# Kernel tuning notes

Hardware: AMD Instinct MI355X
Metric: run time of the kernel (lower is better)

Reference implementation:

```python
import jax, jax.numpy as jnp
import numpy as np

EPS_BN = 1e-3  # nn.BatchNorm1d(num_channels, eps=0.001)
B, C, N = 16, 256, 2048
NUM_SA = 4


def _bn(x, g, b, m, v):
    # eval-mode BatchNorm1d over channel dim of [B, C, N]
    return g[:, None] * (x - m[:, None]) * jax.lax.rsqrt(v[:, None] + EPS_BN) + b[:, None]


def _sa_layer(x, qk_w, v_w, v_b, t_w, t_b, g, b, m, var):
    # q_conv and k_conv share weights -> energy = (Wx)^T (Wx)
    q = jnp.einsum('oc,bcn->bon', qk_w, x)              # [B, C//4, N]
    energy = jnp.einsum('bcm,bcn->bmn', q, q)           # [B, N, N]
    attn = jax.nn.softmax(energy, axis=-1)
    # offset-attention: extra column-sum normalization (dim=1)
    attn = attn / (1e-9 + attn.sum(axis=1, keepdims=True))
    xv = jnp.einsum('oc,bcn->bon', v_w, x) + v_b[:, None]   # [B, C, N]
    x_r = jnp.einsum('bcn,bnm->bcm', xv, attn)              # bmm(x_v, attention)
    t = jnp.einsum('oc,bcn->bon', t_w, x - x_r) + t_b[:, None]
    return x + jax.nn.relu(_bn(t, g, b, m, var))


def setup_inputs() -> dict:
    key = jax.random.key(0)
    ks = jax.random.split(key, 24)
    f32 = jnp.float32
    d = {}
    d['x'] = jax.random.normal(ks[0], (B, C, N), dtype=f32)
    d['conv1_w'] = jax.random.normal(ks[1], (C, C), dtype=f32) * 0.05
    d['conv2_w'] = jax.random.normal(ks[2], (C, C), dtype=f32) * 0.05
    for i, nm in enumerate(['bn1', 'bn2']):
        kk = jax.random.split(ks[3 + i], 4)
        d[nm + '_g'] = 1.0 + 0.05 * jax.random.normal(kk[0], (C,), dtype=f32)
        d[nm + '_b'] = 0.05 * jax.random.normal(kk[1], (C,), dtype=f32)
        d[nm + '_m'] = 0.05 * jax.random.normal(kk[2], (C,), dtype=f32)
        d[nm + '_v'] = jax.random.uniform(kk[3], (C,), dtype=f32, minval=0.5, maxval=1.5)
    d['sa_qk_w'] = jax.random.normal(ks[5], (NUM_SA, C // 4, C), dtype=f32) * 0.05
    d['sa_v_w'] = jax.random.normal(ks[6], (NUM_SA, C, C), dtype=f32) * 0.05
    d['sa_v_b'] = jax.random.normal(ks[7], (NUM_SA, C), dtype=f32) * 0.05
    d['sa_t_w'] = jax.random.normal(ks[8], (NUM_SA, C, C), dtype=f32) * 0.05
    d['sa_t_b'] = jax.random.normal(ks[9], (NUM_SA, C), dtype=f32) * 0.05
    d['sa_g'] = 1.0 + 0.05 * jax.random.normal(ks[10], (NUM_SA, C), dtype=f32)
    d['sa_b'] = 0.05 * jax.random.normal(ks[11], (NUM_SA, C), dtype=f32)
    d['sa_m'] = 0.05 * jax.random.normal(ks[12], (NUM_SA, C), dtype=f32)
    d['sa_var'] = jax.random.uniform(ks[13], (NUM_SA, C), dtype=f32, minval=0.5, maxval=1.5)
    d['flag'] = 0  # False -> primary bn branch
    return d


def reference(x, conv1_w, conv2_w, bn1_g, bn1_b, bn1_m, bn1_v,
              bn2_g, bn2_b, bn2_m, bn2_v,
              sa_qk_w, sa_v_w, sa_v_b, sa_t_w, sa_t_b,
              sa_g, sa_b, sa_m, sa_var, flag):
    h = jax.nn.relu(_bn(jnp.einsum('oc,bcn->bon', conv1_w, x), bn1_g, bn1_b, bn1_m, bn1_v))
    h = jax.nn.relu(_bn(jnp.einsum('oc,bcn->bon', conv2_w, h), bn2_g, bn2_b, bn2_m, bn2_v))
    outs = []
    for i in range(NUM_SA):
        h = _sa_layer(h, sa_qk_w[i], sa_v_w[i], sa_v_b[i], sa_t_w[i], sa_t_b[i],
                      sa_g[i], sa_b[i], sa_m[i], sa_var[i])
        outs.append(h)
    return jnp.concatenate(outs, axis=1)  # [B, 4*C, N]
```

## Files before the change

### kernel.cpp

```cpp
#include <hip/hip_runtime.h>
#include <hip/hip_bf16.h>
#include <hip/hip_fp16.h>

static constexpr int Bn = 16;
static constexpr int Cc = 256;
static constexpr int Nn = 2048;
static constexpr int C4 = 64;
static constexpr float LOG2E = 1.4426950408889634f;

typedef _Float16 half_t;
typedef __attribute__((ext_vector_type(8))) _Float16 half8;
typedef __attribute__((ext_vector_type(4))) _Float16 half4;
typedef __attribute__((ext_vector_type(8))) short short8;
typedef __attribute__((ext_vector_type(4))) float float4v;

static constexpr long sNC = (long)Nn * Cc;
static constexpr long sNQ = (long)Nn * C4;

#define DEVI __device__ __forceinline__

DEVI float bf2f(unsigned short u) { return __uint_as_float(((unsigned)u) << 16); }
DEVI unsigned short f2bf(float f) {
    unsigned x = __float_as_uint(f);
    x += 0x7fffu + ((x >> 16) & 1u);
    return (unsigned short)(x >> 16);
}

DEVI void gload16(const void* g, void* l) {
    __builtin_amdgcn_global_load_lds(
        (const __attribute__((address_space(1))) unsigned int*)g,
        (__attribute__((address_space(3))) unsigned int*)l, 16, 0, 0);
}

enum { EPI_RAW = 0, EPI_H = 1, EPI_XV = 2 };

template<int MODE, int BM, int BN, int WI, int WJ, bool BF16OUT>
__global__ __launch_bounds__(WI * WJ * 64)
void mgemm(const half_t* __restrict__ A, long aB,
           const half_t* __restrict__ Bm, long bB,
           void* __restrict__ Yv, long yB, int ldy,
           const float* __restrict__ bias,
           const float* __restrict__ bng, const float* __restrict__ bnb,
           const float* __restrict__ bnm, const float* __restrict__ bnv,
           int K,
           const float* __restrict__ Pbuf, float* __restrict__ offp)
{
    constexpr int NW = WI * WJ;
    __shared__ __align__(16) half_t Als[2][BM][32];
    __shared__ __align__(16) half_t Bls[2][BN][32];

    const int tid  = threadIdx.x;
    const int w    = tid >> 6;
    const int lane = tid & 63;
    const int wi   = w % WI;
    const int wj   = w / WI;
    const int quad = lane >> 4, m16 = lane & 15;
    const int lr   = lane >> 2, lc = lane & 3;
    const int b    = blockIdx.z;
    const int j0   = blockIdx.x * BN;
    const int i0   = blockIdx.y * BM;

    const half_t* Ab = A + (size_t)b * aB;
    const half_t* Bb = Bm + (size_t)b * bB;

    float4v acc[4][4];
    #pragma unroll
    for (int i = 0; i < 4; ++i)
        #pragma unroll
        for (int j = 0; j < 4; ++j) acc[i][j] = (float4v)0.f;

    bool first = true;
    for (int k0 = 0; k0 < K; k0 += 64) {
        #pragma unroll
        for (int s = 0; s < 2; ++s) {
            const int kk = k0 + s * 32 + lc * 8;
            #pragma unroll
            for (int t = 0; t < BM / (16 * NW); ++t) {
                const int row = (t * NW + w) * 16;
                gload16(Ab + (size_t)(i0 + row + lr) * K + kk, &Als[s][row][0]);
            }
            #pragma unroll
            for (int t = 0; t < BN / (16 * NW); ++t) {
                const int row = (t * NW + w) * 16;
                gload16(Bb + (size_t)(j0 + row + lr) * K + kk, &Bls[s][row][0]);
            }
        }
        if (MODE == EPI_XV && first && Pbuf && tid < 128) {
            const int m = blockIdx.y * 128 + tid;
            const float2* p = (const float2*)(Pbuf + ((size_t)b * Nn + m) * 32);
            float M = -1e30f;
            #pragma unroll
            for (int i = 0; i < 16; ++i) M = fmaxf(M, p[i].x);
            float S = 0.f;
            #pragma unroll
            for (int i = 0; i < 16; ++i) S += p[i].y * __expf(p[i].x - M);
            offp[(size_t)b * Nn + m] = fmaf(M, LOG2E, __log2f(S));
        }
        first = false;
        __syncthreads();
        #pragma unroll
        for (int s = 0; s < 2; ++s) {
            half8 af[4], bf[4];
            #pragma unroll
            for (int t = 0; t < 4; ++t)
                af[t] = *(const half8*)&Als[s][wi * 64 + t * 16 + m16][quad * 8];
            #pragma unroll
            for (int t = 0; t < 4; ++t)
                bf[t] = *(const half8*)&Bls[s][wj * 64 + t * 16 + m16][quad * 8];
            #pragma unroll
            for (int ti = 0; ti < 4; ++ti)
                #pragma unroll
                for (int tj = 0; tj < 4; ++tj)
                    acc[ti][tj] = __builtin_amdgcn_mfma_f32_16x16x32_f16(
                        af[ti], bf[tj], acc[ti][tj], 0, 0, 0);
        }
        __syncthreads();
    }

    #pragma unroll
    for (int ti = 0; ti < 4; ++ti) {
        const int il = i0 + wi * 64 + ti * 16 + quad * 4;
        #pragma unroll
        for (int tj = 0; tj < 4; ++tj) {
            const int jl = j0 + wj * 64 + tj * 16 + m16;
            float4v v = acc[ti][tj];
            if (MODE == EPI_RAW) {
                half4 o;
                #pragma unroll
                for (int r = 0; r < 4; ++r) o[r] = (half_t)v[r];
                *(half4*)((half_t*)Yv + (size_t)b * yB + (size_t)jl * ldy + il) = o;
            } else if (MODE == EPI_H) {
                half4 o;
                #pragma unroll
                for (int r = 0; r < 4; ++r) {
                    const float sc = bng[il + r] * rsqrtf(bnv[il + r] + 1e-3f);
                    const float sh = bnb[il + r] - bnm[il + r] * sc;
                    o[r] = (half_t)fmaxf(fmaf(v[r], sc, sh), 0.f);
                }
                *(half4*)((half_t*)Yv + (size_t)b * yB + (size_t)jl * ldy + il) = o;
            } else {
                const float bj = bias[jl];
                if (BF16OUT) {
                    ushort4 o;
                    o.x = f2bf(v[0] + bj); o.y = f2bf(v[1] + bj);
                    o.z = f2bf(v[2] + bj); o.w = f2bf(v[3] + bj);
                    *(ushort4*)((unsigned short*)Yv + (size_t)b * yB + (size_t)jl * ldy + il) = o;
                } else {
                    half4 o;
                    #pragma unroll
                    for (int r = 0; r < 4; ++r) o[r] = (half_t)(v[r] + bj);
                    *(half4*)((half_t*)Yv + (size_t)b * yB + (size_t)jl * ldy + il) = o;
                }
            }
        }
    }
}

__global__ __launch_bounds__(256)
void estats(const half_t* __restrict__ q, float* __restrict__ Pbuf)
{
    __shared__ __align__(16) half_t sA[128 * 64];
    __shared__ __align__(16) half_t sB[128 * 64];
    __shared__ float red[2][2][4][16][2];
    const int tid = threadIdx.x, w = tid >> 6, lane = tid & 63;
    const int wi = w & 1, wj = w >> 1, quad = lane >> 4, m16 = lane & 15;
    const int f = blockIdx.x;
    const int W = (f & 7) * 512 + (f >> 3);
    const int b = W >> 8;
    const int rem = W & 255;
    const int j0 = (rem & 15) * 128;
    const int ib = rem >> 4;
    const int i0 = ib * 128;
    const half_t* qb = q + (size_t)b * sNQ;

    #pragma unroll
    for (int t = 0; t < 4; ++t) {
        const int g = w * 256 + t * 64 + lane;
        const int r = g >> 3, c = g & 7;
        const int cs = c ^ (r & 7);
        gload16(qb + (size_t)(i0 + r) * 64 + cs * 8, sA + (w * 256 + t * 64) * 8);
        gload16(qb + (size_t)(j0 + r) * 64 + cs * 8, sB + (w * 256 + t * 64) * 8);
    }
    __syncthreads();

    half8 an[4][2], bm[4][2];
    #pragma unroll
    for (int t = 0; t < 4; ++t)
        #pragma unroll
        for (int ks = 0; ks < 2; ++ks) {
            const int pc = ((ks * 4 + quad) ^ (m16 & 7)) * 8;
            an[t][ks] = *(const half8*)&sA[(wi * 64 + t * 16 + m16) * 64 + pc];
            bm[t][ks] = *(const half8*)&sB[(wj * 64 + t * 16 + m16) * 64 + pc];
        }

    #pragma unroll
    for (int tj = 0; tj < 4; ++tj) {
        float4v e[4];
        #pragma unroll
        for (int ti = 0; ti < 4; ++ti) {
            e[ti] = (float4v)0.f;
            e[ti] = __builtin_amdgcn_mfma_f32_16x16x32_f16(an[ti][0], bm[tj][0], e[ti], 0, 0, 0);
            e[ti] = __builtin_amdgcn_mfma_f32_16x16x32_f16(an[ti][1], bm[tj][1], e[ti], 0, 0, 0);
        }
        float lmax = -1e30f;
        #pragma unroll
        for (int ti = 0; ti < 4; ++ti)
            #pragma unroll
            for (int r = 0; r < 4; ++r) lmax = fmaxf(lmax, e[ti][r]);
        lmax = fmaxf(lmax, __shfl_xor(lmax, 16));
        lmax = fmaxf(lmax, __shfl_xor(lmax, 32));
        float ls = 0.f;
        #pragma unroll
        for (int ti = 0; ti < 4; ++ti)
            #pragma unroll
            for (int r = 0; r < 4; ++r) ls += __expf(e[ti][r] - lmax);
        ls += __shfl_xor(ls, 16);
        ls += __shfl_xor(ls, 32);
        if (quad == 0) { red[wi][wj][tj][m16][0] = lmax; red[wi][wj][tj][m16][1] = ls; }
    }
    __syncthreads();
    if (tid < 128) {
        const int wj2 = tid >> 6, tj2 = (tid >> 4) & 3, mm = tid & 15;
        const float m0 = red[0][wj2][tj2][mm][0], s0 = red[0][wj2][tj2][mm][1];
        const float m1 = red[1][wj2][tj2][mm][0], s1 = red[1][wj2][tj2][mm][1];
        const float M = fmaxf(m0, m1);
        const float S = s0 * __expf(m0 - M) + s1 * __expf(m1 - M);
        const int m = j0 + wj2 * 64 + tj2 * 16 + mm;
        *(float2*)(Pbuf + (((size_t)b * Nn + m) * 16 + ib) * 2) = make_float2(M, S);
    }
}

__global__ __launch_bounds__(512)
void flashxr(const half_t* __restrict__ q, const half_t* __restrict__ xv,
             const half_t* __restrict__ h, const float* __restrict__ offp,
             const half_t* __restrict__ tw, const float* __restrict__ tb,
             const float* __restrict__ bng, const float* __restrict__ bnb,
             const float* __restrict__ bnm, const float* __restrict__ bnv,
             float* __restrict__ outL, half_t* __restrict__ hNext,
             const half_t* __restrict__ qkn, half_t* __restrict__ qn)
{
    __shared__ __align__(16) half_t sXV[256 * 64];
    __shared__ __align__(16) half_t sQA[2][64 * 64];
    __shared__ __align__(16) half_t sP[64 * 64];
    __shared__ float sOff[Nn];

    const int tid = threadIdx.x, w = tid >> 6, lane = tid & 63;
    const int quad = lane >> 4, m16 = lane & 15;
    const int wiE = w & 1, wjE = w >> 1;
    const int wi = w & 3, wj = w >> 2;
    const int wjT = w;
    const int f = blockIdx.x;
    const int W = (f & 7) * 64 + (f >> 3);
    const int b = W >> 5, j0 = (W & 31) * 64;
    const half_t* qb  = q + (size_t)b * sNQ;
    const half_t* xvb = xv + (size_t)b * sNC;

    const int sr = tid >> 3, sc = tid & 7;
    const int qsw = (sc ^ (sr & 7)) * 8;

    gload16(qb + (size_t)sr * 64 + qsw, &sQA[0][(size_t)tid * 8]);
    gload16(offp + (size_t)b * Nn + (size_t)tid * 4, sOff + (size_t)tid * 4);

    half8 bq[2];
    #pragma unroll
    for (int s = 0; s < 2; ++s)
        bq[s] = *(const half8*)(qb + (size_t)(j0 + wjE * 16 + m16) * 64 + (s * 4 + quad) * 8);

    __syncthreads();

    float4v acc[4][2];
    #pragma unroll
    for (int i = 0; i < 4; ++i)
        #pragma unroll
        for (int j = 0; j < 2; ++j) acc[i][j] = (float4v)0.f;
    float csa = 0.f;
    const int mrow = wjE * 16 + m16;

    for (int nc = 0; nc < 32; ++nc) {
        #pragma unroll
        for (int t = 0; t < 4; ++t) {
            const int g = t * 512 + tid;
            const int r = g >> 3, c = g & 7;
            gload16(xvb + (size_t)r * Nn + nc * 64 + ((c ^ (r & 7)) * 8),
                    sXV + (size_t)g * 8);
        }
        if (nc < 31)
            gload16(qb + (size_t)((nc + 1) * 64 + sr) * 64 + qsw,
                    &sQA[(nc + 1) & 1][(size_t)tid * 8]);
        __syncthreads();

        const half_t* qA = &sQA[nc & 1][0];
        const int nbase = nc * 64 + wiE * 32 + quad * 4;
        #pragma unroll
        for (int ti = 0; ti < 2; ++ti) {
            const int nl = wiE * 32 + ti * 16 + m16;
            const half8 an0 = *(const half8*)&qA[(size_t)nl * 64 + ((quad ^ (m16 & 7)) * 8)];
            const half8 an1 = *(const half8*)&qA[(size_t)nl * 64 + (((4 + quad) ^ (m16 & 7)) * 8)];
            float4v e = (float4v)0.f;
            e = __builtin_amdgcn_mfma_f32_16x16x32_f16(an0, bq[0], e, 0, 0, 0);
            e = __builtin_amdgcn_mfma_f32_16x16x32_f16(an1, bq[1], e, 0, 0, 0);
            const float4v o4 = *(const float4v*)&sOff[nbase + ti * 16];
            float c0 = 0.f; ushort4 pk;
            #pragma unroll
            for (int r = 0; r < 4; ++r) {
                const float p = __builtin_amdgcn_exp2f(fmaf(e[r], LOG2E, -o4[r]));
                c0 += p; (&pk.x)[r] = f2bf(p);
            }
            csa += c0;
            const int pc = (wiE * 4 + ti * 2 + (quad >> 1)) ^ (m16 & 7);
            *(ushort4*)&((unsigned short*)sP)[(size_t)mrow * 64 + pc * 8 + (quad & 1) * 4] = pk;
        }
        __syncthreads();

        #pragma unroll
        for (int ks = 0; ks < 2; ++ks) {
            short8 xa[4], pb[2];
            #pragma unroll
            for (int ti = 0; ti < 4; ++ti)
                xa[ti] = *(const short8*)&sXV[(size_t)(wi * 64 + ti * 16 + m16) * 64
                                              + (((ks * 4 + quad) ^ (m16 & 7)) * 8)];
            #pragma unroll
            for (int tj = 0; tj < 2; ++tj)
                pb[tj] = *(const short8*)&sP[(size_t)(wj * 32 + tj * 16 + m16) * 64
                                             + (((ks * 4 + quad) ^ (m16 & 7)) * 8)];
            __builtin_amdgcn_s_setprio(1);
            #pragma unroll
            for (int ti = 0; ti < 4; ++ti)
                #pragma unroll
                for (int tj = 0; tj < 2; ++tj)
                    acc[ti][tj] = __builtin_amdgcn_mfma_f32_16x16x32_bf16(
                        xa[ti], pb[tj], acc[ti][tj], 0, 0, 0);
            __builtin_amdgcn_s_setprio(0);
        }
        __syncthreads();
    }

    csa += __shfl_xor(csa, 16);
    csa += __shfl_xor(csa, 32);
    float* fb = (float*)sP;
    if (lane < 16) fb[wiE * 64 + wjE * 16 + lane] = csa;
    __syncthreads();
    float csr[2];
    #pragma unroll
    for (int tj = 0; tj < 2; ++tj) {
        const int m = wj * 32 + tj * 16 + m16;
        csr[tj] = 1.0f / (1e-9f + fb[m] + fb[64 + m]);
    }

    const half_t* hb = h + (size_t)b * sNC;
    half_t* sD = sXV;
    #pragma unroll
    for (int ti = 0; ti < 4; ++ti) {
        const int cg = wi * 64 + ti * 16 + quad * 4;
        const int cc = (cg >> 3) ^ (m16 & 7);
        const int sub = (quad & 1) * 4;
        #pragma unroll
        for (int tj = 0; tj < 2; ++tj) {
            const int mr = wj * 32 + tj * 16 + m16;
            const int mg = j0 + mr;
            const half4 hv = *(const half4*)&hb[(size_t)mg * Cc + cg];
            half4 o;
            #pragma unroll
            for (int r = 0; r < 4; ++r)
                o[r] = (half_t)((float)hv[r] - acc[ti][tj][r] * csr[tj]);
            *(half4*)&sD[(size_t)mr * 256 + cc * 8 + sub] = o;
        }
    }
    __syncthreads();

    float4v acc2[4][2];
    #pragma unroll
    for (int i = 0; i < 4; ++i)
        #pragma unroll
        for (int j = 0; j < 2; ++j) acc2[i][j] = (float4v)0.f;
    #pragma unroll
    for (int ks = 0; ks < 8; ++ks) {
        half8 af[4], bf[2];
        #pragma unroll
        for (int tm = 0; tm < 4; ++tm)
            af[tm] = *(const half8*)&sD[(size_t)(tm * 16 + m16) * 256
                                        + (((ks * 4 + quad) ^ (m16 & 7)) * 8)];
        #pragma unroll
        for (int tc = 0; tc < 2; ++tc)
            bf[tc] = *(const half8*)&tw[(size_t)(wjT * 32 + tc * 16 + m16) * 256
                                        + ks * 32 + quad * 8];
        #pragma unroll
        for (int tm = 0; tm < 4; ++tm)
            #pragma unroll
            for (int tc = 0; tc < 2; ++tc)
                acc2[tm][tc] = __builtin_amdgcn_mfma_f32_16x16x32_f16(
                    af[tm], bf[tc], acc2[tm][tc], 0, 0, 0);
    }

    if (qn) __syncthreads();

    half_t* sH = sXV;
    const long yB = (long)4 * Cc * Nn;
    float* yb = outL + (size_t)b * yB;
    half_t* hn = hNext ? hNext + (size_t)b * sNC : nullptr;
    #pragma unroll
    for (int tc = 0; tc < 2; ++tc) {
        const int co = wjT * 32 + tc * 16 + m16;
        const float tb2 = tb[co];
        const float sc2 = bng[co] * rsqrtf(bnv[co] + 1e-3f);
        const float sh2 = bnb[co] - bnm[co] * sc2;
        #pragma unroll
        for (int tm = 0; tm < 4; ++tm) {
            const int mg = j0 + tm * 16 + quad * 4;
            float4v o;
            #pragma unroll
            for (int r = 0; r < 4; ++r) {
                const float t2  = acc2[tm][tc][r] + tb2;
                const float rel = fmaxf(fmaf(t2, sc2, sh2), 0.f);
                const float hv  = (float)hb[(size_t)(mg + r) * Cc + co];
                const float ov  = hv + rel;
                o[r] = ov;
                if (hn) hn[(size_t)(mg + r) * Cc + co] = (half_t)ov;
                if (qn) {
                    const int row = tm * 16 + quad * 4 + r;
                    const int chk = ((co >> 3) ^ (row & 7));
                    sH[(size_t)row * 256 + chk * 8 + (co & 7)] = (half_t)ov;
                }
            }
            *(float4v*)&yb[(size_t)co * Nn + mg] = o;
        }
    }

    if (qn) {
        __syncthreads();
        const int ot = w & 3;
        const int mt0 = (w >> 2) * 2;
        float4v acc3[2];
        acc3[0] = (float4v)0.f; acc3[1] = (float4v)0.f;
        #pragma unroll
        for (int ks = 0; ks < 8; ++ks) {
            const half8 bf = *(const half8*)&qkn[(size_t)(ot * 16 + m16) * 256
                                                + ks * 32 + quad * 8];
            #pragma unroll
            for (int mi = 0; mi < 2; ++mi) {
                const half8 af = *(const half8*)&sH[(size_t)((mt0 + mi) * 16 + m16) * 256
                                                    + (((ks * 4 + quad) ^ (m16 & 7)) * 8)];
                acc3[mi] = __builtin_amdgcn_mfma_f32_16x16x32_f16(af, bf, acc3[mi], 0, 0, 0);
            }
        }
        half_t* qnb = qn + (size_t)b * sNQ;
        #pragma unroll
        for (int mi = 0; mi < 2; ++mi)
            #pragma unroll
            for (int r = 0; r < 4; ++r)
                qnb[(size_t)(j0 + (mt0 + mi) * 16 + quad * 4 + r) * 64
                    + ot * 16 + m16] = (half_t)acc3[mi][r];
    }
}

__global__ __launch_bounds__(256)
void xpose_cast(const float* __restrict__ x, half_t* __restrict__ xT)
{
    __shared__ half_t tile[32][33];
    const int tx = threadIdx.x & 31, ty = threadIdx.x >> 5;
    const int n0 = blockIdx.x * 32, c0 = blockIdx.y * 32, b = blockIdx.z;
    #pragma unroll
    for (int r = 0; r < 4; ++r)
        tile[ty * 4 + r][tx] =
            (half_t)x[((size_t)b * Cc + c0 + ty * 4 + r) * Nn + n0 + tx];
    __syncthreads();
    #pragma unroll
    for (int r = 0; r < 4; ++r)
        xT[((size_t)b * Nn + n0 + ty * 4 + r) * Cc + c0 + tx] = tile[tx][ty * 4 + r];
}

__global__ __launch_bounds__(256)
void castall(const float* __restrict__ c1, const float* __restrict__ c2,
             const float* __restrict__ qk, const float* __restrict__ vw,
             const float* __restrict__ tw, half_t* __restrict__ dst)
{
    const int i = (blockIdx.x * 256 + threadIdx.x) * 4;
    const float* s; int o;
    if      (i < 65536)  { s = c1; o = 0; }
    else if (i < 131072) { s = c2; o = 65536; }
    else if (i < 196608) { s = qk; o = 131072; }
    else if (i < 458752) { s = vw; o = 196608; }
    else                 { s = tw; o = 458752; }
    const float4v v = *(const float4v*)(s + (i - o));
    half4 out;
    #pragma unroll
    for (int r = 0; r < 4; ++r) out[r] = (half_t)v[r];
    *(half4*)(dst + i) = out;
}

extern "C" void kernel_launch(void* const* d_in, const int* in_sizes, int n_in,
                              void* d_out, int out_size, void* d_ws, size_t ws_size,
                              hipStream_t stream)
{
    const float* x    = (const float*)d_in[0];
    const float* c1w  = (const float*)d_in[1];
    const float* c2w  = (const float*)d_in[2];
    const float* bn1g = (const float*)d_in[3], *bn1b = (const float*)d_in[4];
    const float* bn1m = (const float*)d_in[5], *bn1v = (const float*)d_in[6];
    const float* bn2g = (const float*)d_in[7], *bn2b = (const float*)d_in[8];
    const float* bn2m = (const float*)d_in[9], *bn2v = (const float*)d_in[10];
    const float* qkw  = (const float*)d_in[11];
    const float* vw   = (const float*)d_in[12];
    const float* vb   = (const float*)d_in[13];
    const float* tw   = (const float*)d_in[14];
    const float* tb   = (const float*)d_in[15];
    const float* sag  = (const float*)d_in[16];
    const float* sab  = (const float*)d_in[17];
    const float* sam  = (const float*)d_in[18];
    const float* sav  = (const float*)d_in[19];
    float* out = (float*)d_out;

    char* ws = (char*)d_ws;
    const size_t HSZ = (size_t)Bn * Nn * Cc * 2;
    half_t* xT   = (half_t*)(ws);
    half_t* hA   = (half_t*)(ws + HSZ);
    half_t* hBuf = (half_t*)(ws + 2 * HSZ);
    half_t* q_sA = (half_t*)(ws + 3 * HSZ);
    half_t* xv_s = (half_t*)(ws + 3 * HSZ + (size_t)4194304);
    float*  Pbuf = (float*) (ws + 4 * HSZ + (size_t)4194304);
    float*  offp = (float*) (ws + 4 * HSZ + (size_t)8388608);
    half_t* warena = (half_t*)(ws + 4 * HSZ + (size_t)8519680);
    half_t* q_sB = (half_t*)(ws + 4 * HSZ + (size_t)8519680 + (size_t)2097152);
    half_t* wc1  = warena;
    half_t* wc2  = wc1 + 65536;
    half_t* wqk  = wc2 + 65536;
    half_t* wv   = wqk + 65536;
    half_t* wt   = wv  + 262144;

    dim3 blk(256);

    castall<<<768, blk, 0, stream>>>(c1w, c2w, qkw, vw, tw, warena);
    xpose_cast<<<dim3(Nn / 32, Cc / 32, Bn), blk, 0, stream>>>(x, xT);

    mgemm<EPI_H, 256, 128, 4, 2, false><<<dim3(16, 1, Bn), dim3(512), 0, stream>>>(
        wc1, 0, xT, sNC, hA, sNC, Cc,
        nullptr, bn1g, bn1b, bn1m, bn1v, Cc, nullptr, nullptr);
    mgemm<EPI_H, 256, 128, 4, 2, false><<<dim3(16, 1, Bn), dim3(512), 0, stream>>>(
        wc2, 0, hA, sNC, hBuf, sNC, Cc,
        nullptr, bn2g, bn2b, bn2m, bn2v, Cc, nullptr, nullptr);

    mgemm<EPI_RAW, 64, 256, 1, 4, false><<<dim3(8, 1, Bn), blk, 0, stream>>>(
        wqk, 0, hBuf, sNC, q_sA, sNQ, C4,
        nullptr, nullptr, nullptr, nullptr, nullptr, Cc, nullptr, nullptr);

    half_t* hcur = hBuf;
    half_t* hnxt = hA;
    half_t* qcur = q_sA;
    half_t* qnxt = q_sB;
    for (int L = 0; L < 4; ++L) {
        estats<<<dim3(4096), blk, 0, stream>>>(qcur, Pbuf);
        mgemm<EPI_XV, 128, 256, 2, 4, true><<<dim3(1, 16, Bn), dim3(512), 0, stream>>>(
            hcur, sNC, wv + (long)L * Cc * Cc, 0, xv_s, (long)Cc * Nn, Nn,
            vb + L * Cc, nullptr, nullptr, nullptr, nullptr, Cc, Pbuf, offp);
        flashxr<<<dim3(512), dim3(512), 0, stream>>>(
            qcur, xv_s, hcur, offp,
            wt + (long)L * Cc * Cc, tb + L * Cc,
            sag + L * Cc, sab + L * Cc, sam + L * Cc, sav + L * Cc,
            out + (long)L * Cc * Nn, (L < 3) ? hnxt : nullptr,
            wqk + (long)(L + 1 < 4 ? L + 1 : 0) * C4 * Cc,
            (L < 3) ? qnxt : nullptr);
        half_t* tmp = hcur; hcur = hnxt; hnxt = tmp;
        half_t* tq  = qcur; qcur = qnxt; qnxt = tq;
    }
}
```

Baseline: 671.5 us.

## Merge softmax-stats and value-projection GEMM into one heterogeneous kernel launch

Fuses the estats kernel and the xv GEMM into a single launch, estxv, whose first 256 blocks compute the value projection and whose remaining 2048 blocks compute the energy row-block max/sum statistics. The stats blocks now cover 256 rows each with 512 threads. The final reduction of the partial stats into a log-sum-exp offset moves into the flashxr prologue, which reads Pbuf directly, so the separate offp buffer is removed. This saves one launch per layer and lets the two independent workloads share the GPU. The cost is that every flashxr block repeats the offset reduction for its whole batch.

```diff
diff --git a/kernel.cpp b/kernel.cpp
--- a/kernel.cpp
+++ b/kernel.cpp
@@ -32,18 +32,16 @@
         (__attribute__((address_space(3))) unsigned int*)l, 16, 0, 0);
 }
 
-enum { EPI_RAW = 0, EPI_H = 1, EPI_XV = 2 };
-
-template<int MODE, int BM, int BN, int WI, int WJ, bool BF16OUT>
+enum { EPI_RAW = 0, EPI_H = 1 };
+
+template<int MODE, int BM, int BN, int WI, int WJ>
 __global__ __launch_bounds__(WI * WJ * 64)
 void mgemm(const half_t* __restrict__ A, long aB,
            const half_t* __restrict__ Bm, long bB,
            void* __restrict__ Yv, long yB, int ldy,
-           const float* __restrict__ bias,
            const float* __restrict__ bng, const float* __restrict__ bnb,
            const float* __restrict__ bnm, const float* __restrict__ bnv,
-           int K,
-           const float* __restrict__ Pbuf, float* __restrict__ offp)
+           int K)
 {
     constexpr int NW = WI * WJ;
     __shared__ __align__(16) half_t Als[2][BM][32];
@@ -69,7 +67,6 @@
         #pragma unroll
         for (int j = 0; j < 4; ++j) acc[i][j] = (float4v)0.f;
 
-    bool first = true;
     for (int k0 = 0; k0 < K; k0 += 64) {
         #pragma unroll
         for (int s = 0; s < 2; ++s) {
@@ -85,18 +82,6 @@
                 gload16(Bb + (size_t)(j0 + row + lr) * K + kk, &Bls[s][row][0]);
             }
         }
-        if (MODE == EPI_XV && first && Pbuf && tid < 128) {
-            const int m = blockIdx.y * 128 + tid;
-            const float2* p = (const float2*)(Pbuf + ((size_t)b * Nn + m) * 32);
-            float M = -1e30f;
-            #pragma unroll
-            for (int i = 0; i < 16; ++i) M = fmaxf(M, p[i].x);
-            float S = 0.f;
-            #pragma unroll
-            for (int i = 0; i < 16; ++i) S += p[i].y * __expf(p[i].x - M);
-            offp[(size_t)b * Nn + m] = fmaf(M, LOG2E, __log2f(S));
-        }
-        first = false;
         __syncthreads();
         #pragma unroll
         for (int s = 0; s < 2; ++s) {
@@ -129,7 +114,7 @@
                 #pragma unroll
                 for (int r = 0; r < 4; ++r) o[r] = (half_t)v[r];
                 *(half4*)((half_t*)Yv + (size_t)b * yB + (size_t)jl * ldy + il) = o;
-            } else if (MODE == EPI_H) {
+            } else {
                 half4 o;
                 #pragma unroll
                 for (int r = 0; r < 4; ++r) {
@@ -138,101 +123,176 @@
                     o[r] = (half_t)fmaxf(fmaf(v[r], sc, sh), 0.f);
                 }
                 *(half4*)((half_t*)Yv + (size_t)b * yB + (size_t)jl * ldy + il) = o;
-            } else {
-                const float bj = bias[jl];
-                if (BF16OUT) {
-                    ushort4 o;
-                    o.x = f2bf(v[0] + bj); o.y = f2bf(v[1] + bj);
-                    o.z = f2bf(v[2] + bj); o.w = f2bf(v[3] + bj);
-                    *(ushort4*)((unsigned short*)Yv + (size_t)b * yB + (size_t)jl * ldy + il) = o;
-                } else {
-                    half4 o;
+            }
+        }
+    }
+}
+
+__global__ __launch_bounds__(512)
+void estxv(const half_t* __restrict__ q, float* __restrict__ Pbuf,
+           const half_t* __restrict__ h, const half_t* __restrict__ vw,
+           const float* __restrict__ vb, unsigned short* __restrict__ xv)
+{
+    __shared__ __align__(16) char smem[57344];
+
+    const int tid = threadIdx.x, w = tid >> 6, lane = tid & 63;
+    const int quad = lane >> 4, m16 = lane & 15;
+
+    if (blockIdx.x < 256) {
+        half_t (*Als)[128][32] = (half_t(*)[128][32])smem;
+        half_t (*Bls)[256][32] = (half_t(*)[256][32])(smem + 16384);
+        const int f2 = blockIdx.x;
+        const int W2 = (f2 & 7) * 32 + (f2 >> 3);
+        const int b = W2 >> 4, i0 = (W2 & 15) * 128;
+        const int wi = w & 1, wj = w >> 1;
+        const int lr = lane >> 2, lc = lane & 3;
+        const half_t* Ab = h + (size_t)b * sNC;
+
+        float4v acc[4][4];
+        #pragma unroll
+        for (int i = 0; i < 4; ++i)
+            #pragma unroll
+            for (int j = 0; j < 4; ++j) acc[i][j] = (float4v)0.f;
+
+        for (int k0 = 0; k0 < Cc; k0 += 64) {
+            #pragma unroll
+            for (int s = 0; s < 2; ++s) {
+                const int kk = k0 + s * 32 + lc * 8;
+                {
+                    const int row = w * 16;
+                    gload16(Ab + (size_t)(i0 + row + lr) * Cc + kk, &Als[s][row][0]);
+                }
+                #pragma unroll
+                for (int t = 0; t < 2; ++t) {
+                    const int row = (t * 8 + w) * 16;
+                    gload16(vw + (size_t)(row + lr) * Cc + kk, &Bls[s][row][0]);
+                }
+            }
+            __syncthreads();
+            #pragma unroll
+            for (int s = 0; s < 2; ++s) {
+                half8 af[4], bf[4];
+                #pragma unroll
+                for (int t = 0; t < 4; ++t)
+                    af[t] = *(const half8*)&Als[s][wi * 64 + t * 16 + m16][quad * 8];
+                #pragma unroll
+                for (int t = 0; t < 4; ++t)
+                    bf[t] = *(const half8*)&Bls[s][wj * 64 + t * 16 + m16][quad * 8];
+                #pragma unroll
+                for (int ti = 0; ti < 4; ++ti)
                     #pragma unroll
-                    for (int r = 0; r < 4; ++r) o[r] = (half_t)(v[r] + bj);
-                    *(half4*)((half_t*)Yv + (size_t)b * yB + (size_t)jl * ldy + il) = o;
-                }
-            }
-        }
-    }
-}
-
-__global__ __launch_bounds__(256)
-void estats(const half_t* __restrict__ q, float* __restrict__ Pbuf)
-{
-    __shared__ __align__(16) half_t sA[128 * 64];
-    __shared__ __align__(16) half_t sB[128 * 64];
-    __shared__ float red[2][2][4][16][2];
-    const int tid = threadIdx.x, w = tid >> 6, lane = tid & 63;
-    const int wi = w & 1, wj = w >> 1, quad = lane >> 4, m16 = lane & 15;
-    const int f = blockIdx.x;
-    const int W = (f & 7) * 512 + (f >> 3);
-    const int b = W >> 8;
-    const int rem = W & 255;
-    const int j0 = (rem & 15) * 128;
-    const int ib = rem >> 4;
-    const int i0 = ib * 128;
-    const half_t* qb = q + (size_t)b * sNQ;
-
-    #pragma unroll
-    for (int t = 0; t < 4; ++t) {
-        const int g = w * 256 + t * 64 + lane;
-        const int r = g >> 3, c = g & 7;
-        const int cs = c ^ (r & 7);
-        gload16(qb + (size_t)(i0 + r) * 64 + cs * 8, sA + (w * 256 + t * 64) * 8);
-        gload16(qb + (size_t)(j0 + r) * 64 + cs * 8, sB + (w * 256 + t * 64) * 8);
-    }
-    __syncthreads();
-
-    half8 an[4][2], bm[4][2];
-    #pragma unroll
-    for (int t = 0; t < 4; ++t)
-        #pragma unroll
-        for (int ks = 0; ks < 2; ++ks) {
-            const int pc = ((ks * 4 + quad) ^ (m16 & 7)) * 8;
-            an[t][ks] = *(const half8*)&sA[(wi * 64 + t * 16 + m16) * 64 + pc];
-            bm[t][ks] = *(const half8*)&sB[(wj * 64 + t * 16 + m16) * 64 + pc];
-        }
-
-    #pragma unroll
-    for (int tj = 0; tj < 4; ++tj) {
-        float4v e[4];
+                    for (int tj = 0; tj < 4; ++tj)
+                        acc[ti][tj] = __builtin_amdgcn_mfma_f32_16x16x32_f16(
+                            af[ti], bf[tj], acc[ti][tj], 0, 0, 0);
+            }
+            __syncthreads();
+        }
+
         #pragma unroll
         for (int ti = 0; ti < 4; ++ti) {
-            e[ti] = (float4v)0.f;
-            e[ti] = __builtin_amdgcn_mfma_f32_16x16x32_f16(an[ti][0], bm[tj][0], e[ti], 0, 0, 0);
-            e[ti] = __builtin_amdgcn_mfma_f32_16x16x32_f16(an[ti][1], bm[tj][1], e[ti], 0, 0, 0);
-        }
-        float lmax = -1e30f;
-        #pragma unroll
-        for (int ti = 0; ti < 4; ++ti)
-            #pragma unroll
-            for (int r = 0; r < 4; ++r) lmax = fmaxf(lmax, e[ti][r]);
-        lmax = fmaxf(lmax, __shfl_xor(lmax, 16));
-        lmax = fmaxf(lmax, __shfl_xor(lmax, 32));
-        float ls = 0.f;
-        #pragma unroll
-        for (int ti = 0; ti < 4; ++ti)
-            #pragma unroll
-            for (int r = 0; r < 4; ++r) ls += __expf(e[ti][r] - lmax);
-        ls += __shfl_xor(ls, 16);
-        ls += __shfl_xor(ls, 32);
-        if (quad == 0) { red[wi][wj][tj][m16][0] = lmax; red[wi][wj][tj][m16][1] = ls; }
-    }
-    __syncthreads();
-    if (tid < 128) {
-        const int wj2 = tid >> 6, tj2 = (tid >> 4) & 3, mm = tid & 15;
-        const float m0 = red[0][wj2][tj2][mm][0], s0 = red[0][wj2][tj2][mm][1];
-        const float m1 = red[1][wj2][tj2][mm][0], s1 = red[1][wj2][tj2][mm][1];
-        const float M = fmaxf(m0, m1);
-        const float S = s0 * __expf(m0 - M) + s1 * __expf(m1 - M);
-        const int m = j0 + wj2 * 64 + tj2 * 16 + mm;
-        *(float2*)(Pbuf + (((size_t)b * Nn + m) * 16 + ib) * 2) = make_float2(M, S);
+            const int il = i0 + wi * 64 + ti * 16 + quad * 4;
+            #pragma unroll
+            for (int tj = 0; tj < 4; ++tj) {
+                const int jl = wj * 64 + tj * 16 + m16;
+                const float bj = vb[jl];
+                float4v v = acc[ti][tj];
+                ushort4 o;
+                o.x = f2bf(v[0] + bj); o.y = f2bf(v[1] + bj);
+                o.z = f2bf(v[2] + bj); o.w = f2bf(v[3] + bj);
+                *(ushort4*)(xv + (size_t)b * sNC + (size_t)jl * Nn + il) = o;
+            }
+        }
+    } else {
+        half_t* sA = (half_t*)smem;
+        half_t* sB = (half_t*)(smem + 32768);
+        float*  red = (float*)(smem + 49152);
+        #define RIDX(ih_, wi_, wj_, tj_, mm_) \
+            ((((((ih_) * 2 + (wi_)) * 2 + (wj_)) * 4 + (tj_)) * 16 + (mm_)) * 2)
+        const int f = blockIdx.x - 256;
+        const int ih = w >> 2, w4 = w & 3;
+        const int wi = w4 & 1, wj = w4 >> 1;
+        const int W = (f & 7) * 256 + (f >> 3);
+        const int b = W >> 7;
+        const int rem = W & 127;
+        const int j0 = (rem & 15) * 128;
+        const int ip = rem >> 4;
+        const int i0 = ip * 256;
+        const half_t* qb = q + (size_t)b * sNQ;
+
+        #pragma unroll
+        for (int t = 0; t < 4; ++t) {
+            const int g = t * 512 + tid;
+            const int r = g >> 3, c = g & 7;
+            gload16(qb + (size_t)(i0 + r) * 64 + ((c ^ (r & 7)) * 8), sA + (size_t)g * 8);
+        }
+        #pragma unroll
+        for (int t = 0; t < 2; ++t) {
+            const int g = t * 512 + tid;
+            const int r = g >> 3, c = g & 7;
+            gload16(qb + (size_t)(j0 + r) * 64 + ((c ^ (r & 7)) * 8), sB + (size_t)g * 8);
+        }
+        __syncthreads();
+
+        half8 an[4][2], bm[4][2];
+        #pragma unroll
+        for (int t = 0; t < 4; ++t)
+            #pragma unroll
+            for (int ks = 0; ks < 2; ++ks) {
+                const int pc = ((ks * 4 + quad) ^ (m16 & 7)) * 8;
+                an[t][ks] = *(const half8*)&sA[(size_t)(ih * 128 + wi * 64 + t * 16 + m16) * 64 + pc];
+                bm[t][ks] = *(const half8*)&sB[(size_t)(wj * 64 + t * 16 + m16) * 64 + pc];
+            }
+
+        #pragma unroll
+        for (int tj = 0; tj < 4; ++tj) {
+            float4v e[4];
+            #pragma unroll
+            for (int ti = 0; ti < 4; ++ti) {
+                e[ti] = (float4v)0.f;
+                e[ti] = __builtin_amdgcn_mfma_f32_16x16x32_f16(an[ti][0], bm[tj][0], e[ti], 0, 0, 0);
+                e[ti] = __builtin_amdgcn_mfma_f32_16x16x32_f16(an[ti][1], bm[tj][1], e[ti], 0, 0, 0);
+            }
+            float lmax = -1e30f;
+            #pragma unroll
+            for (int ti = 0; ti < 4; ++ti)
+                #pragma unroll
+                for (int r = 0; r < 4; ++r) lmax = fmaxf(lmax, e[ti][r]);
+            lmax = fmaxf(lmax, __shfl_xor(lmax, 16));
+            lmax = fmaxf(lmax, __shfl_xor(lmax, 32));
+            float ls = 0.f;
+            #pragma unroll
+            for (int ti = 0; ti < 4; ++ti)
+                #pragma unroll
+                for (int r = 0; r < 4; ++r) ls += __expf(e[ti][r] - lmax);
+            ls += __shfl_xor(ls, 16);
+            ls += __shfl_xor(ls, 32);
+            if (quad == 0) {
+                red[RIDX(ih, wi, wj, tj, m16) + 0] = lmax;
+                red[RIDX(ih, wi, wj, tj, m16) + 1] = ls;
+            }
+        }
+        __syncthreads();
+        if (tid < 256) {
+            const int ih2 = tid >> 7;
+            const int t7 = tid & 127;
+            const int wj2 = t7 >> 6, tj2 = (t7 >> 4) & 3, mm = t7 & 15;
+            const float m0 = red[RIDX(ih2, 0, wj2, tj2, mm) + 0];
+            const float s0 = red[RIDX(ih2, 0, wj2, tj2, mm) + 1];
+            const float m1 = red[RIDX(ih2, 1, wj2, tj2, mm) + 0];
+            const float s1 = red[RIDX(ih2, 1, wj2, tj2, mm) + 1];
+            const float M = fmaxf(m0, m1);
+            const float S = s0 * __expf(m0 - M) + s1 * __expf(m1 - M);
+            const int m = j0 + wj2 * 64 + tj2 * 16 + mm;
+            *(float2*)(Pbuf + (((size_t)b * Nn + m) * 16 + ip * 2 + ih2) * 2)
+                = make_float2(M, S);
+        }
+        #undef RIDX
     }
 }
 
 __global__ __launch_bounds__(512)
 void flashxr(const half_t* __restrict__ q, const half_t* __restrict__ xv,
-             const half_t* __restrict__ h, const float* __restrict__ offp,
+             const half_t* __restrict__ h, const float* __restrict__ Pbuf,
              const half_t* __restrict__ tw, const float* __restrict__ tb,
              const float* __restrict__ bng, const float* __restrict__ bnb,
              const float* __restrict__ bnm, const float* __restrict__ bnv,
@@ -259,13 +319,33 @@
     const int qsw = (sc ^ (sr & 7)) * 8;
 
     gload16(qb + (size_t)sr * 64 + qsw, &sQA[0][(size_t)tid * 8]);
-    gload16(offp + (size_t)b * Nn + (size_t)tid * 4, sOff + (size_t)tid * 4);
 
     half8 bq[2];
     #pragma unroll
     for (int s = 0; s < 2; ++s)
         bq[s] = *(const half8*)(qb + (size_t)(j0 + wjE * 16 + m16) * 64 + (s * 4 + quad) * 8);
 
+    {
+        const float* pB = Pbuf + (size_t)b * Nn * 32;
+        #pragma unroll
+        for (int ii = 0; ii < 4; ++ii) {
+            const int i = ii * 512 + tid;
+            const float4v* p4 = (const float4v*)(pB + (size_t)i * 32);
+            float4v v[8];
+            #pragma unroll
+            for (int t = 0; t < 8; ++t) v[t] = p4[t];
+            float M = -1e30f;
+            #pragma unroll
+            for (int t = 0; t < 8; ++t) { M = fmaxf(M, v[t][0]); M = fmaxf(M, v[t][2]); }
+            float S = 0.f;
+            #pragma unroll
+            for (int t = 0; t < 8; ++t) {
+                S += v[t][1] * __expf(v[t][0] - M);
+                S += v[t][3] * __expf(v[t][2] - M);
+            }
+            sOff[i] = fmaf(M, LOG2E, __log2f(S));
+        }
+    }
     __syncthreads();
 
     float4v acc[4][2];
@@ -518,7 +598,6 @@
     half_t* q_sA = (half_t*)(ws + 3 * HSZ);
     half_t* xv_s = (half_t*)(ws + 3 * HSZ + (size_t)4194304);
     float*  Pbuf = (float*) (ws + 4 * HSZ + (size_t)4194304);
-    float*  offp = (float*) (ws + 4 * HSZ + (size_t)8388608);
     half_t* warena = (half_t*)(ws + 4 * HSZ + (size_t)8519680);
     half_t* q_sB = (half_t*)(ws + 4 * HSZ + (size_t)8519680 + (size_t)2097152);
     half_t* wc1  = warena;
@@ -532,28 +611,25 @@
     castall<<<768, blk, 0, stream>>>(c1w, c2w, qkw, vw, tw, warena);
     xpose_cast<<<dim3(Nn / 32, Cc / 32, Bn), blk, 0, stream>>>(x, xT);
 
-    mgemm<EPI_H, 256, 128, 4, 2, false><<<dim3(16, 1, Bn), dim3(512), 0, stream>>>(
-        wc1, 0, xT, sNC, hA, sNC, Cc,
-        nullptr, bn1g, bn1b, bn1m, bn1v, Cc, nullptr, nullptr);
-    mgemm<EPI_H, 256, 128, 4, 2, false><<<dim3(16, 1, Bn), dim3(512), 0, stream>>>(
-        wc2, 0, hA, sNC, hBuf, sNC, Cc,
-        nullptr, bn2g, bn2b, bn2m, bn2v, Cc, nullptr, nullptr);
-
-    mgemm<EPI_RAW, 64, 256, 1, 4, false><<<dim3(8, 1, Bn), blk, 0, stream>>>(
+    mgemm<EPI_H, 256, 128, 4, 2><<<dim3(16, 1, Bn), dim3(512), 0, stream>>>(
+        wc1, 0, xT, sNC, hA, sNC, Cc, bn1g, bn1b, bn1m, bn1v, Cc);
+    mgemm<EPI_H, 256, 128, 4, 2><<<dim3(16, 1, Bn), dim3(512), 0, stream>>>(
+        wc2, 0, hA, sNC, hBuf, sNC, Cc, bn2g, bn2b, bn2m, bn2v, Cc);
+
+    mgemm<EPI_RAW, 64, 256, 1, 4><<<dim3(8, 1, Bn), blk, 0, stream>>>(
         wqk, 0, hBuf, sNC, q_sA, sNQ, C4,
-        nullptr, nullptr, nullptr, nullptr, nullptr, Cc, nullptr, nullptr);
+        nullptr, nullptr, nullptr, nullptr, Cc);
 
     half_t* hcur = hBuf;
     half_t* hnxt = hA;
     half_t* qcur = q_sA;
     half_t* qnxt = q_sB;
     for (int L = 0; L < 4; ++L) {
-        estats<<<dim3(4096), blk, 0, stream>>>(qcur, Pbuf);
-        mgemm<EPI_XV, 128, 256, 2, 4, true><<<dim3(1, 16, Bn), dim3(512), 0, stream>>>(
-            hcur, sNC, wv + (long)L * Cc * Cc, 0, xv_s, (long)Cc * Nn, Nn,
-            vb + L * Cc, nullptr, nullptr, nullptr, nullptr, Cc, Pbuf, offp);
+        estxv<<<dim3(2304), dim3(512), 0, stream>>>(
+            qcur, Pbuf, hcur, wv + (long)L * Cc * Cc, vb + L * Cc,
+            (unsigned short*)xv_s);
         flashxr<<<dim3(512), dim3(512), 0, stream>>>(
-            qcur, xv_s, hcur, offp,
+            qcur, xv_s, hcur, Pbuf,
             wt + (long)L * Cc * Cc, tb + L * Cc,
             sag + L * Cc, sab + L * Cc, sam + L * Cc, sav + L * Cc,
             out + (long)L * Cc * Nn, (L < 3) ? hnxt : nullptr,
```

New measurement: 732.2 us. 1.09x slower.
